# Kernel optimization log

Hardware: AMD Instinct MI355X
Metric: run time of the kernel (lower is better)

The kernel has to match this reference:

```python
import jax, jax.numpy as jnp
import numpy as np

B, S, H, D = 4, 2048, 8, 64


def init_offset(size, a=0.02, b=0.1, lo=8.0, hi=14.0):
    if size == 1:
        return jnp.array([(hi - lo) / 2], dtype=jnp.float32)
    x = jnp.log(jnp.expm1(jnp.linspace(a, b, size)))
    x = (x - x.min()) / (x.max() - x.min())
    return (x * abs(hi - lo) + lo).astype(jnp.float32)


def setup_inputs() -> dict:
    key = jax.random.key(0)
    k1, k2, k3 = jax.random.split(key, 3)
    qk = jax.random.normal(k1, (B, S, 2, H, D), dtype=jnp.float32)
    v = jax.random.normal(k2, (B, S, H, D), dtype=jnp.float32)
    n = jax.random.normal(k3, (B, S, H), dtype=jnp.float32)
    offset = init_offset(H)  # learned per-head offset parameter
    return {"qk": qk, "v": v, "n": n, "offset": offset}


def reference(qk, v, n, offset):
    # approx_fn = elu(x) + 1 (feature map), norm_fn = softplus, scale_B=True
    q = jax.nn.elu(qk[:, :, 0]) + 1.0  # (B,S,H,D)
    k = jax.nn.elu(qk[:, :, 1]) + 1.0  # (B,S,H,D)
    scale = 1.0 / jnp.sqrt(jnp.asarray(q.shape[-1], q.dtype))
    # outer product per position then causal prefix-sum over sequence
    kv = jnp.einsum('bshd,bsht->bshdt', k * scale, v)  # (B,S,H,D,D)
    kv = jnp.cumsum(kv, axis=1)
    out = jnp.einsum('bshd,bshdt->bsht', q, kv)  # (B,S,H,D)
    norm = jnp.exp(-jax.nn.softplus(n + offset))  # (B,S,H)
    return norm[:, :, :, None] * out
```

## Files before the change

kernel.cpp:

```cpp
#include <hip/hip_runtime.h>
#include <cstdint>

#define BB 4
#define SS 2048
#define HH 8
#define DD 64
#define CC 64
#define NCK (SS/CC)
#define BHH (BB*HH)

typedef __attribute__((ext_vector_type(8))) short  short8;
typedef __attribute__((ext_vector_type(4))) float  f32x4;
typedef __attribute__((ext_vector_type(4))) unsigned short us4;

__device__ __forceinline__ float elu1(float x) {
    return x > 0.f ? x + 1.f : __expf(x);
}
__device__ __forceinline__ unsigned short f2bf(float f) {
    unsigned int u = __float_as_uint(f);
    u += 0x7FFFu + ((u >> 16) & 1u);
    return (unsigned short)(u >> 16);
}
__device__ __forceinline__ int swz(int r, int c) { return r * 64 + (c ^ ((r & 7) << 3)); }

__global__ __launch_bounds__(256) void kv_chunk_kernel(
    const float* __restrict__ qk, const float* __restrict__ v,
    float* __restrict__ kvws)
{
    const int blk = blockIdx.x;
    const int bh = blk / NCK, c = blk % NCK;
    const int b = bh / HH, h = bh % HH;
    const int s0 = c * CC;

    __shared__ float kb[CC * DD];
    __shared__ float vb[CC * DD];

    for (int i = threadIdx.x; i < CC * DD; i += 256) {
        const int s = i >> 6, d = i & 63;
        const float kraw = qk[(((size_t)(b * SS + s0 + s) * 2 + 1) * HH + h) * DD + d];
        kb[i] = elu1(kraw) * 0.125f;
        vb[i] = v[((size_t)(b * SS + s0 + s) * HH + h) * DD + d];
    }
    __syncthreads();

    const int ty = threadIdx.x >> 4;
    const int tx = threadIdx.x & 15;

    float acc[4][4] = {};
    for (int s = 0; s < CC; ++s) {
        float vr[4], kr[4];
#pragma unroll
        for (int i = 0; i < 4; ++i) {
            vr[i] = vb[s * DD + ty * 4 + i];
            kr[i] = kb[s * DD + tx * 4 + i];
        }
#pragma unroll
        for (int i = 0; i < 4; ++i)
#pragma unroll
            for (int j = 0; j < 4; ++j)
                acc[i][j] += vr[i] * kr[j];
    }

    float* dst = kvws + (size_t)blk * (DD * DD);
#pragma unroll
    for (int i = 0; i < 4; ++i) {
        float4 t = make_float4(acc[i][0], acc[i][1], acc[i][2], acc[i][3]);
        *reinterpret_cast<float4*>(dst + (ty * 4 + i) * DD + tx * 4) = t;
    }
}

__global__ __launch_bounds__(256) void prefix_kernel(float* __restrict__ kvws)
{
    const int bh = blockIdx.x >> 4, part = blockIdx.x & 15;
    const int e = part * 256 + threadIdx.x;
    float* p = kvws + (size_t)bh * NCK * (DD * DD) + e;

    float vals[NCK];
#pragma unroll
    for (int c = 0; c < NCK; ++c) vals[c] = p[(size_t)c * (DD * DD)];
    float run = 0.f;
#pragma unroll
    for (int c = 0; c < NCK; ++c) {
        const float t = vals[c];
        p[(size_t)c * (DD * DD)] = run;
        run += t;
    }
}

__global__ __launch_bounds__(256) void out_kernel(
    const float* __restrict__ qk, const float* __restrict__ v,
    const float* __restrict__ nrm, const float* __restrict__ offset,
    const float* __restrict__ kvws, float* __restrict__ out)
{
    const int blk = blockIdx.x;
    const int bh = blk / NCK, c = blk % NCK;
    const int b = bh / HH, h = bh % HH;
    const int s0 = c * CC;

    __shared__ unsigned short qb[CC * DD];
    __shared__ unsigned short kb[CC * DD];
    __shared__ unsigned short st[CC * DD];

    const int tid = threadIdx.x;
    const float* stg = kvws + (size_t)blk * (DD * DD);

    for (int it = tid; it < 1024; it += 256) {
        const int r = it >> 4;
        const int c0 = (it & 15) * 4;
        const size_t qrow = (((size_t)(b * SS + s0 + r) * 2 + 0) * HH + h) * DD;
        const size_t krow = (((size_t)(b * SS + s0 + r) * 2 + 1) * HH + h) * DD;

        float4 fq = *reinterpret_cast<const float4*>(qk + qrow + c0);
        us4 uq; uq.x = f2bf(elu1(fq.x)); uq.y = f2bf(elu1(fq.y));
                uq.z = f2bf(elu1(fq.z)); uq.w = f2bf(elu1(fq.w));
        *reinterpret_cast<us4*>(&qb[swz(r, c0)]) = uq;

        float4 fk = *reinterpret_cast<const float4*>(qk + krow + c0);
        us4 uk; uk.x = f2bf(elu1(fk.x) * 0.125f); uk.y = f2bf(elu1(fk.y) * 0.125f);
                uk.z = f2bf(elu1(fk.z) * 0.125f); uk.w = f2bf(elu1(fk.w) * 0.125f);
        *reinterpret_cast<us4*>(&kb[swz(r, c0)]) = uk;

        float4 fs = *reinterpret_cast<const float4*>(stg + r * DD + c0);
        us4 us_; us_.x = f2bf(fs.x); us_.y = f2bf(fs.y);
                 us_.z = f2bf(fs.z); us_.w = f2bf(fs.w);
        *reinterpret_cast<us4*>(&st[swz(r, c0)]) = us_;
    }
    __syncthreads();

    const int lane  = tid & 63;
    const int wid   = tid >> 6;
    const int lr    = lane & 15;
    const int lk    = (lane >> 4) * 8;
    const int mbase = wid * 16;
    const int crow  = (lane >> 4) * 4;

    short8 aq0 = *reinterpret_cast<const short8*>(&qb[swz(mbase + lr, lk)]);
    short8 aq1 = *reinterpret_cast<const short8*>(&qb[swz(mbase + lr, 32 + lk)]);

    f32x4 acc[4] = {};
    f32x4 as4[4] = {};

#pragma unroll
    for (int kk = 0; kk < 2; ++kk) {
        const short8 aq = kk ? aq1 : aq0;
#pragma unroll
        for (int nb = 0; nb < 4; ++nb) {
            short8 bs = *reinterpret_cast<const short8*>(&st[swz(nb * 16 + lr, kk * 32 + lk)]);
            acc[nb] = __builtin_amdgcn_mfma_f32_16x16x32_bf16(aq, bs, acc[nb], 0, 0, 0);
            short8 bk = *reinterpret_cast<const short8*>(&kb[swz(nb * 16 + lr, kk * 32 + lk)]);
            as4[nb] = __builtin_amdgcn_mfma_f32_16x16x32_bf16(aq, bk, as4[nb], 0, 0, 0);
        }
    }

    __syncthreads();

#pragma unroll
    for (int nb = 0; nb < 4; ++nb) {
#pragma unroll
        for (int r = 0; r < 4; ++r) {
            const int s_loc = mbase + crow + r;
            const int s2    = nb * 16 + lr;
            const float val = (s2 <= s_loc) ? as4[nb][r] : 0.f;
            st[swz(s_loc, s2)] = f2bf(val);
        }
    }
    __syncthreads();

    short8 aA0 = *reinterpret_cast<const short8*>(&st[swz(mbase + lr, lk)]);
    short8 aA1 = *reinterpret_cast<const short8*>(&st[swz(mbase + lr, 32 + lk)]);
    const float* vbase = v + ((size_t)(b * SS + s0) * HH + h) * DD;

#pragma unroll
    for (int kk = 0; kk < 2; ++kk) {
        const short8 aa = kk ? aA1 : aA0;
        short8 bvf[4];
#pragma unroll
        for (int nb = 0; nb < 4; ++nb) {
            const float* vp = vbase + (size_t)(kk * 32 + lk) * (HH * DD) + nb * 16 + lr;
#pragma unroll
            for (int j = 0; j < 8; ++j)
                bvf[nb][j] = (short)f2bf(vp[(size_t)j * (HH * DD)]);
        }
#pragma unroll
        for (int nb = 0; nb < 4; ++nb)
            acc[nb] = __builtin_amdgcn_mfma_f32_16x16x32_bf16(aa, bvf[nb], acc[nb], 0, 0, 0);
    }

    const float off = offset[h];
    float nv[4];
#pragma unroll
    for (int r = 0; r < 4; ++r) {
        const int s = s0 + mbase + crow + r;
        nv[r] = 1.f / (1.f + __expf(nrm[(size_t)(b * SS + s) * HH + h] + off));
    }
#pragma unroll
    for (int nb = 0; nb < 4; ++nb) {
#pragma unroll
        for (int r = 0; r < 4; ++r) {
            const int s = s0 + mbase + crow + r;
            out[((size_t)(b * SS + s) * HH + h) * DD + nb * 16 + lr] = acc[nb][r] * nv[r];
        }
    }
}

extern "C" void kernel_launch(void* const* d_in, const int* in_sizes, int n_in,
                              void* d_out, int out_size, void* d_ws, size_t ws_size,
                              hipStream_t stream) {
    const float* qk     = (const float*)d_in[0];
    const float* v      = (const float*)d_in[1];
    const float* nrm    = (const float*)d_in[2];
    const float* offset = (const float*)d_in[3];
    float* out  = (float*)d_out;
    float* kvws = (float*)d_ws;

    kv_chunk_kernel<<<dim3(BHH * NCK), dim3(256), 0, stream>>>(qk, v, kvws);
    prefix_kernel<<<dim3(BHH * 16), dim3(256), 0, stream>>>(kvws);
    out_kernel<<<dim3(BHH * NCK), dim3(256), 0, stream>>>(qk, v, nrm, offset, kvws, out);
}
```

Baseline: 125.1 us.

## Use MFMA for chunk KV states and store bf16 state and transposed V

The per-chunk K^T V product moves from scalar FMAs to bf16 MFMA, with K and V transposed in shared memory through lane shuffles. The chunk states and the prefix scan workspace become bf16 instead of fp32, which halves workspace traffic. V is also written once as a transposed bf16 tile, so the output kernel can read it with vector loads instead of strided scalar global loads. The cost is lower precision in the accumulated prefix states, since each running sum is rounded to bf16.

```diff
diff --git a/kernel.cpp b/kernel.cpp
--- a/kernel.cpp
+++ b/kernel.cpp
@@ -21,76 +21,131 @@
     u += 0x7FFFu + ((u >> 16) & 1u);
     return (unsigned short)(u >> 16);
 }
-__device__ __forceinline__ int swz(int r, int c) { return r * 64 + (c ^ ((r & 7) << 3)); }
+__device__ __forceinline__ float bf2f(unsigned short h) {
+    return __uint_as_float(((unsigned int)h) << 16);
+}
+#define SWZ(r,c) ((r) * DD + ((c) ^ (((r) & 7) << 3)))
+
+template<int M0, int M1>
+__device__ __forceinline__ void xpose4(float v[4], int lane) {
+    {
+        const bool hi = (lane & M0) != 0;
+        float x0 = hi ? v[0] : v[1];
+        float x1 = hi ? v[2] : v[3];
+        float r0 = __shfl_xor(x0, M0);
+        float r1 = __shfl_xor(x1, M0);
+        if (hi) { v[0] = r0; v[2] = r1; } else { v[1] = r0; v[3] = r1; }
+    }
+    {
+        const bool hi = (lane & M1) != 0;
+        float x0 = hi ? v[0] : v[2];
+        float x1 = hi ? v[1] : v[3];
+        float r0 = __shfl_xor(x0, M1);
+        float r1 = __shfl_xor(x1, M1);
+        if (hi) { v[0] = r0; v[1] = r1; } else { v[2] = r0; v[3] = r1; }
+    }
+}
+
+__device__ __forceinline__ unsigned long long pack4bf(const float v[4]) {
+    unsigned long long r;
+    r  = (unsigned long long)f2bf(v[0]);
+    r |= (unsigned long long)f2bf(v[1]) << 16;
+    r |= (unsigned long long)f2bf(v[2]) << 32;
+    r |= (unsigned long long)f2bf(v[3]) << 48;
+    return r;
+}
 
 __global__ __launch_bounds__(256) void kv_chunk_kernel(
     const float* __restrict__ qk, const float* __restrict__ v,
-    float* __restrict__ kvws)
+    unsigned short* __restrict__ Sws, unsigned short* __restrict__ vtws)
 {
     const int blk = blockIdx.x;
     const int bh = blk / NCK, c = blk % NCK;
     const int b = bh / HH, h = bh % HH;
     const int s0 = c * CC;
 
-    __shared__ float kb[CC * DD];
-    __shared__ float vb[CC * DD];
-
-    for (int i = threadIdx.x; i < CC * DD; i += 256) {
-        const int s = i >> 6, d = i & 63;
-        const float kraw = qk[(((size_t)(b * SS + s0 + s) * 2 + 1) * HH + h) * DD + d];
-        kb[i] = elu1(kraw) * 0.125f;
-        vb[i] = v[((size_t)(b * SS + s0 + s) * HH + h) * DD + d];
-    }
-    __syncthreads();
-
-    const int ty = threadIdx.x >> 4;
-    const int tx = threadIdx.x & 15;
-
-    float acc[4][4] = {};
-    for (int s = 0; s < CC; ++s) {
-        float vr[4], kr[4];
-#pragma unroll
-        for (int i = 0; i < 4; ++i) {
-            vr[i] = vb[s * DD + ty * 4 + i];
-            kr[i] = kb[s * DD + tx * 4 + i];
-        }
-#pragma unroll
-        for (int i = 0; i < 4; ++i)
-#pragma unroll
-            for (int j = 0; j < 4; ++j)
-                acc[i][j] += vr[i] * kr[j];
-    }
-
-    float* dst = kvws + (size_t)blk * (DD * DD);
-#pragma unroll
-    for (int i = 0; i < 4; ++i) {
-        float4 t = make_float4(acc[i][0], acc[i][1], acc[i][2], acc[i][3]);
-        *reinterpret_cast<float4*>(dst + (ty * 4 + i) * DD + tx * 4) = t;
-    }
-}
-
-__global__ __launch_bounds__(256) void prefix_kernel(float* __restrict__ kvws)
+    __shared__ unsigned short kT[CC * DD];
+    __shared__ unsigned short vT[CC * DD];
+
+    const int tid = threadIdx.x, lane = tid & 63;
+
+#pragma unroll
+    for (int iter = 0; iter < 4; ++iter) {
+        const int it = iter * 256 + tid;
+        const int r = it >> 4, c0 = (it & 15) * 4;
+        const int g = lane >> 4;
+        const int rb = r - g;
+
+        float4 fk = *reinterpret_cast<const float4*>(
+            qk + (((size_t)(b * SS + s0 + r) * 2 + 1) * HH + h) * DD + c0);
+        float kv4[4] = { elu1(fk.x) * 0.125f, elu1(fk.y) * 0.125f,
+                         elu1(fk.z) * 0.125f, elu1(fk.w) * 0.125f };
+        xpose4<16, 32>(kv4, lane);
+        *reinterpret_cast<unsigned long long*>(&kT[SWZ(c0 + g, rb)]) = pack4bf(kv4);
+
+        float4 fv = *reinterpret_cast<const float4*>(
+            v + ((size_t)(b * SS + s0 + r) * HH + h) * DD + c0);
+        float vv4[4] = { fv.x, fv.y, fv.z, fv.w };
+        xpose4<16, 32>(vv4, lane);
+        *reinterpret_cast<unsigned long long*>(&vT[SWZ(c0 + g, rb)]) = pack4bf(vv4);
+    }
+    __syncthreads();
+
+#pragma unroll
+    for (int j = 0; j < 2; ++j) {
+        const int slot = j * 256 + tid;
+        const int r = slot >> 3, c0 = (slot & 7) * 8;
+        short8 val = *reinterpret_cast<const short8*>(&vT[SWZ(r, c0)]);
+        *reinterpret_cast<short8*>(vtws + (size_t)blk * 4096 + slot * 8) = val;
+    }
+
+    const int lr = lane & 15, lk = (lane >> 4) * 8;
+    const int wid = tid >> 6, mbase = wid * 16;
+    f32x4 acc[4] = {};
+#pragma unroll
+    for (int kk = 0; kk < 2; ++kk) {
+        short8 a = *reinterpret_cast<const short8*>(&vT[SWZ(mbase + lr, kk * 32 + lk)]);
+#pragma unroll
+        for (int nb = 0; nb < 4; ++nb) {
+            short8 bk = *reinterpret_cast<const short8*>(&kT[SWZ(nb * 16 + lr, kk * 32 + lk)]);
+            acc[nb] = __builtin_amdgcn_mfma_f32_16x16x32_bf16(a, bk, acc[nb], 0, 0, 0);
+        }
+    }
+
+    const int crow = (lane >> 4) * 4;
+#pragma unroll
+    for (int nb = 0; nb < 4; ++nb) {
+        float cv[4] = { acc[nb][0], acc[nb][1], acc[nb][2], acc[nb][3] };
+        xpose4<1, 2>(cv, lane);
+        const int t  = mbase + crow + (lane & 3);
+        const int d0 = nb * 16 + (lr & ~3);
+        *reinterpret_cast<unsigned long long*>(
+            Sws + (size_t)blk * 4096 + t * 64 + d0) = pack4bf(cv);
+    }
+}
+
+__global__ __launch_bounds__(256) void prefix_kernel(unsigned short* __restrict__ Sws)
 {
     const int bh = blockIdx.x >> 4, part = blockIdx.x & 15;
     const int e = part * 256 + threadIdx.x;
-    float* p = kvws + (size_t)bh * NCK * (DD * DD) + e;
-
-    float vals[NCK];
-#pragma unroll
-    for (int c = 0; c < NCK; ++c) vals[c] = p[(size_t)c * (DD * DD)];
+    unsigned short* p = Sws + (size_t)bh * NCK * 4096 + e;
+
+    unsigned short vals[NCK];
+#pragma unroll
+    for (int c = 0; c < NCK; ++c) vals[c] = p[(size_t)c * 4096];
     float run = 0.f;
 #pragma unroll
     for (int c = 0; c < NCK; ++c) {
-        const float t = vals[c];
-        p[(size_t)c * (DD * DD)] = run;
-        run += t;
+        p[(size_t)c * 4096] = f2bf(run);
+        run += bf2f(vals[c]);
     }
 }
 
 __global__ __launch_bounds__(256) void out_kernel(
-    const float* __restrict__ qk, const float* __restrict__ v,
-    const float* __restrict__ nrm, const float* __restrict__ offset,
-    const float* __restrict__ kvws, float* __restrict__ out)
+    const float* __restrict__ qk, const float* __restrict__ nrm,
+    const float* __restrict__ offset,
+    const unsigned short* __restrict__ Sws, const unsigned short* __restrict__ vtws,
+    float* __restrict__ out)
 {
     const int blk = blockIdx.x;
     const int bh = blk / NCK, c = blk % NCK;
@@ -100,30 +155,35 @@
     __shared__ unsigned short qb[CC * DD];
     __shared__ unsigned short kb[CC * DD];
     __shared__ unsigned short st[CC * DD];
+    __shared__ unsigned short vt[CC * DD];
 
     const int tid = threadIdx.x;
-    const float* stg = kvws + (size_t)blk * (DD * DD);
-
-    for (int it = tid; it < 1024; it += 256) {
-        const int r = it >> 4;
-        const int c0 = (it & 15) * 4;
+
+#pragma unroll
+    for (int iter = 0; iter < 4; ++iter) {
+        const int it = iter * 256 + tid;
+        const int r = it >> 4, c0 = (it & 15) * 4;
         const size_t qrow = (((size_t)(b * SS + s0 + r) * 2 + 0) * HH + h) * DD;
         const size_t krow = (((size_t)(b * SS + s0 + r) * 2 + 1) * HH + h) * DD;
 
         float4 fq = *reinterpret_cast<const float4*>(qk + qrow + c0);
         us4 uq; uq.x = f2bf(elu1(fq.x)); uq.y = f2bf(elu1(fq.y));
                 uq.z = f2bf(elu1(fq.z)); uq.w = f2bf(elu1(fq.w));
-        *reinterpret_cast<us4*>(&qb[swz(r, c0)]) = uq;
+        *reinterpret_cast<us4*>(&qb[SWZ(r, c0)]) = uq;
 
         float4 fk = *reinterpret_cast<const float4*>(qk + krow + c0);
         us4 uk; uk.x = f2bf(elu1(fk.x) * 0.125f); uk.y = f2bf(elu1(fk.y) * 0.125f);
                 uk.z = f2bf(elu1(fk.z) * 0.125f); uk.w = f2bf(elu1(fk.w) * 0.125f);
-        *reinterpret_cast<us4*>(&kb[swz(r, c0)]) = uk;
-
-        float4 fs = *reinterpret_cast<const float4*>(stg + r * DD + c0);
-        us4 us_; us_.x = f2bf(fs.x); us_.y = f2bf(fs.y);
-                 us_.z = f2bf(fs.z); us_.w = f2bf(fs.w);
-        *reinterpret_cast<us4*>(&st[swz(r, c0)]) = us_;
+        *reinterpret_cast<us4*>(&kb[SWZ(r, c0)]) = uk;
+    }
+#pragma unroll
+    for (int j = 0; j < 2; ++j) {
+        const int slot = j * 256 + tid;
+        const int r = slot >> 3, c0 = (slot & 7) * 8;
+        *reinterpret_cast<short8*>(&st[SWZ(r, c0)]) =
+            *reinterpret_cast<const short8*>(Sws + (size_t)blk * 4096 + slot * 8);
+        *reinterpret_cast<short8*>(&vt[SWZ(r, c0)]) =
+            *reinterpret_cast<const short8*>(vtws + (size_t)blk * 4096 + slot * 8);
     }
     __syncthreads();
 
@@ -134,8 +194,8 @@
     const int mbase = wid * 16;
     const int crow  = (lane >> 4) * 4;
 
-    short8 aq0 = *reinterpret_cast<const short8*>(&qb[swz(mbase + lr, lk)]);
-    short8 aq1 = *reinterpret_cast<const short8*>(&qb[swz(mbase + lr, 32 + lk)]);
+    short8 aq0 = *reinterpret_cast<const short8*>(&qb[SWZ(mbase + lr, lk)]);
+    short8 aq1 = *reinterpret_cast<const short8*>(&qb[SWZ(mbase + lr, 32 + lk)]);
 
     f32x4 acc[4] = {};
     f32x4 as4[4] = {};
@@ -145,9 +205,9 @@
         const short8 aq = kk ? aq1 : aq0;
 #pragma unroll
         for (int nb = 0; nb < 4; ++nb) {
-            short8 bs = *reinterpret_cast<const short8*>(&st[swz(nb * 16 + lr, kk * 32 + lk)]);
+            short8 bs = *reinterpret_cast<const short8*>(&st[SWZ(nb * 16 + lr, kk * 32 + lk)]);
             acc[nb] = __builtin_amdgcn_mfma_f32_16x16x32_bf16(aq, bs, acc[nb], 0, 0, 0);
-            short8 bk = *reinterpret_cast<const short8*>(&kb[swz(nb * 16 + lr, kk * 32 + lk)]);
+            short8 bk = *reinterpret_cast<const short8*>(&kb[SWZ(nb * 16 + lr, kk * 32 + lk)]);
             as4[nb] = __builtin_amdgcn_mfma_f32_16x16x32_bf16(aq, bk, as4[nb], 0, 0, 0);
         }
     }
@@ -161,29 +221,21 @@
             const int s_loc = mbase + crow + r;
             const int s2    = nb * 16 + lr;
             const float val = (s2 <= s_loc) ? as4[nb][r] : 0.f;
-            st[swz(s_loc, s2)] = f2bf(val);
-        }
-    }
-    __syncthreads();
-
-    short8 aA0 = *reinterpret_cast<const short8*>(&st[swz(mbase + lr, lk)]);
-    short8 aA1 = *reinterpret_cast<const short8*>(&st[swz(mbase + lr, 32 + lk)]);
-    const float* vbase = v + ((size_t)(b * SS + s0) * HH + h) * DD;
-
+            st[SWZ(s_loc, s2)] = f2bf(val);
+        }
+    }
+    __syncthreads();
+
+    short8 aA0 = *reinterpret_cast<const short8*>(&st[SWZ(mbase + lr, lk)]);
+    short8 aA1 = *reinterpret_cast<const short8*>(&st[SWZ(mbase + lr, 32 + lk)]);
 #pragma unroll
     for (int kk = 0; kk < 2; ++kk) {
         const short8 aa = kk ? aA1 : aA0;
-        short8 bvf[4];
 #pragma unroll
         for (int nb = 0; nb < 4; ++nb) {
-            const float* vp = vbase + (size_t)(kk * 32 + lk) * (HH * DD) + nb * 16 + lr;
-#pragma unroll
-            for (int j = 0; j < 8; ++j)
-                bvf[nb][j] = (short)f2bf(vp[(size_t)j * (HH * DD)]);
-        }
-#pragma unroll
-        for (int nb = 0; nb < 4; ++nb)
-            acc[nb] = __builtin_amdgcn_mfma_f32_16x16x32_bf16(aa, bvf[nb], acc[nb], 0, 0, 0);
+            short8 bv = *reinterpret_cast<const short8*>(&vt[SWZ(nb * 16 + lr, kk * 32 + lk)]);
+            acc[nb] = __builtin_amdgcn_mfma_f32_16x16x32_bf16(aa, bv, acc[nb], 0, 0, 0);
+        }
     }
 
     const float off = offset[h];
@@ -210,10 +262,12 @@
     const float* v      = (const float*)d_in[1];
     const float* nrm    = (const float*)d_in[2];
     const float* offset = (const float*)d_in[3];
-    float* out  = (float*)d_out;
-    float* kvws = (float*)d_ws;
-
-    kv_chunk_kernel<<<dim3(BHH * NCK), dim3(256), 0, stream>>>(qk, v, kvws);
-    prefix_kernel<<<dim3(BHH * 16), dim3(256), 0, stream>>>(kvws);
-    out_kernel<<<dim3(BHH * NCK), dim3(256), 0, stream>>>(qk, v, nrm, offset, kvws, out);
-}
+    float* out = (float*)d_out;
+
+    unsigned short* Sws  = (unsigned short*)d_ws;
+    unsigned short* vtws = Sws + (size_t)BHH * NCK * 4096;
+
+    kv_chunk_kernel<<<dim3(BHH * NCK), dim3(256), 0, stream>>>(qk, v, Sws, vtws);
+    prefix_kernel<<<dim3(BHH * 16), dim3(256), 0, stream>>>(Sws);
+    out_kernel<<<dim3(BHH * NCK), dim3(256), 0, stream>>>(qk, nrm, offset, Sws, vtws, out);
+}
```

Result: faster. 110.3 us (-11.8%).
